# Performance work log

Measured on AMD Instinct MI355X. Metric: run time of the kernel, lower is better.

## Reference

```python
import jax, jax.numpy as jnp
import numpy as np

NHID = 512
T_K, T_Q, B = 256, 128, 8


def setup_inputs() -> dict:
    key = jax.random.key(0)
    k1, k2, k3, k4, k5 = jax.random.split(key, 5)
    query = jax.random.normal(k1, (T_Q, B, NHID), dtype=jnp.float32)
    c_key = jax.random.normal(k2, (T_K, B, NHID), dtype=jnp.float32)
    mask = jax.random.randint(k3, (T_K, B), 0, 2).astype(bool)
    # att_mlp params: Linear(2*nhid, nhid) -> Tanh -> Linear(nhid, 1)
    # stored as [in, out] so y = x @ W + b (torch Linear weight transposed)
    W1 = jax.random.normal(k4, (2 * NHID, NHID), dtype=jnp.float32) / np.sqrt(2 * NHID)
    b1 = jnp.zeros((NHID,), dtype=jnp.float32)
    W2 = jax.random.normal(k5, (NHID, 1), dtype=jnp.float32) / np.sqrt(NHID)
    b2 = jnp.zeros((1,), dtype=jnp.float32)
    return {"query": query, "c_key": c_key, "mask": mask,
            "W1": W1, "b1": b1, "W2": W2, "b2": b2}


def reference(query, c_key, mask, W1, b1, W2, b2):
    H = query.shape[-1]
    # cat([k_expand, q_expand], -1) @ W1 == k @ W1[:H] + q @ W1[H:]
    # (avoids materializing the [T_k, T_q, B, 2H] concat the torch code builds)
    k_proj = jnp.einsum('kbh,hd->kbd', c_key, W1[:H])   # [T_k, B, H]
    q_proj = jnp.einsum('qbh,hd->qbd', query, W1[H:])   # [T_q, B, H]
    h = jnp.tanh(k_proj[:, None, :, :] + q_proj[None, :, :, :] + b1)  # [T_k, T_q, B, H]
    att_score = jnp.einsum('kqbh,ho->kqb', h, W2) + b2[0]             # [T_k, T_q, B]
    att_score = jnp.where(mask[:, None, :], -jnp.inf, att_score)
    att_prob = jax.nn.softmax(att_score, axis=0)                      # softmax over keys
    # c_val defaults to c_key in the original forward
    ant_vec = jnp.einsum('kqb,kbh->qbh', att_prob, c_key)             # [T_q, B, H]
    return ant_vec, att_prob
```

## Files before the change

### kernel.cpp

```cpp
#include <hip/hip_runtime.h>
#include <math.h>

#define NHID 512
#define T_K  256
#define T_Q  128
#define BB   8

constexpr float C2L2E = 2.8853900817779268f;
constexpr float L2E   = 1.4426950408889634f;

__device__ __forceinline__ float fexp2(float x) { return __builtin_amdgcn_exp2f(x); }
__device__ __forceinline__ float frcp(float x)  { return __builtin_amdgcn_rcpf(x); }

typedef __attribute__((ext_vector_type(8))) short bf16x8;
typedef __attribute__((ext_vector_type(4))) float f32x4;
typedef __attribute__((ext_vector_type(2))) float f32x2;
typedef __attribute__((ext_vector_type(4))) float f32x4v;

__device__ __forceinline__ f32x2 fma2(f32x2 a, f32x2 b, f32x2 c) {
    return __builtin_elementwise_fma(a, b, c);
}

__device__ __forceinline__ unsigned short f2bf(float x) {
    unsigned u = __builtin_bit_cast(unsigned, x);
    unsigned r = (u + 0x7FFFu + ((u >> 16) & 1u)) >> 16;
    return (unsigned short)r;
}
__device__ __forceinline__ float bf2f(unsigned short h) {
    unsigned u = ((unsigned)h) << 16;
    return __builtin_bit_cast(float, u);
}
__device__ __forceinline__ unsigned packbf(float a, float b) {
    return (unsigned)f2bf(a) | ((unsigned)f2bf(b) << 16);
}
__device__ __forceinline__ float lo16(unsigned u) {
    return __builtin_bit_cast(float, u << 16);
}
__device__ __forceinline__ float hi16(unsigned u) {
    return __builtin_bit_cast(float, u & 0xFFFF0000u);
}

__global__ __launch_bounds__(256) void proj_kernel(
    const float* __restrict__ qry, const float* __restrict__ ckey,
    const float* __restrict__ W1, const float* __restrict__ b1,
    uint4* __restrict__ ekto, float* __restrict__ eq,
    unsigned int* __restrict__ ckp)
{
    const int row0 = blockIdx.x * 32;
    const int col0 = blockIdx.y * 64;
    const bool isK = row0 < 2048;
    const int bhalf = isK ? 0 : 512;

    __shared__ __align__(16) unsigned short As_h[32 * 64];
    __shared__ __align__(16) unsigned short As_l[32 * 64];
    __shared__ __align__(16) unsigned short Bs_h[64 * 64];
    __shared__ __align__(16) unsigned short Bs_l[64 * 64];

    const int t    = threadIdx.x;
    const int wave = t >> 6;
    const int lane = t & 63;
    const int wm = (wave & 1) * 16;
    const int wn = (wave >> 1) * 32;

    f32x4 acc[2] = {};

    const int srA = t >> 3;
    const int scA = (t & 7) * 8;
    const float* gA = (isK ? ckey + (size_t)(row0 + srA) * 512
                           : qry  + (size_t)(row0 - 2048 + srA) * 512) + scA;
    const int swA = ((scA >> 3) ^ (srA & 7)) * 8;
    const bool emit_ckp = isK && (col0 == 0);
    const int rowA = row0 + srA;
    unsigned int* ckp_dst = emit_ckp
        ? ckp + ((size_t)(rowA & 7) * 256 + (rowA >> 3)) * 256
        : nullptr;

    const int nB = t & 63;
    const int kgB = wave * 16;
    const float* gB = W1 + (size_t)(bhalf + kgB) * 512 + col0 + nB;
    const int caB = wave * 2;
    const int swB0 = nB * 64 + (((caB + 0) ^ (nB & 7)) * 8);
    const int swB1 = nB * 64 + (((caB + 1) ^ (nB & 7)) * 8);

    const int quad = lane >> 4, fr = lane & 15;

    float4 pa0 = *(const float4*)&gA[0];
    float4 pa1 = *(const float4*)&gA[4];
    float bv[16];
    #pragma unroll
    for (int kk = 0; kk < 16; ++kk)
        bv[kk] = gB[(size_t)kk * 512];

    for (int k0 = 0; k0 < 512; k0 += 64) {
        float fa[8];
        *(float4*)&fa[0] = pa0; *(float4*)&fa[4] = pa1;
        union { uint4 v; unsigned short s[8]; } hA, lA, bh0, bh1, bl0, bl1;
        #pragma unroll
        for (int e = 0; e < 8; ++e) {
            const unsigned short hb = f2bf(fa[e]);
            hA.s[e] = hb; lA.s[e] = f2bf(fa[e] - bf2f(hb));
        }
        #pragma unroll
        for (int e = 0; e < 8; ++e) {
            const unsigned short hb = f2bf(bv[e]);
            bh0.s[e] = hb; bl0.s[e] = f2bf(bv[e] - bf2f(hb));
        }
        #pragma unroll
        for (int e = 0; e < 8; ++e) {
            const unsigned short hb = f2bf(bv[8 + e]);
            bh1.s[e] = hb; bl1.s[e] = f2bf(bv[8 + e] - bf2f(hb));
        }
        if (emit_ckp)
            *(uint4*)&ckp_dst[(k0 + scA) >> 1] = hA.v;

        __syncthreads();
        *(uint4*)&As_h[srA * 64 + swA] = hA.v;
        *(uint4*)&As_l[srA * 64 + swA] = lA.v;
        *(uint4*)&Bs_h[swB0] = bh0.v;  *(uint4*)&Bs_h[swB1] = bh1.v;
        *(uint4*)&Bs_l[swB0] = bl0.v;  *(uint4*)&Bs_l[swB1] = bl1.v;
        __syncthreads();

        if (k0 + 64 < 512) {
            pa0 = *(const float4*)&gA[k0 + 64];
            pa1 = *(const float4*)&gA[k0 + 68];
            #pragma unroll
            for (int kk = 0; kk < 16; ++kk)
                bv[kk] = gB[(size_t)(k0 + 64 + kk) * 512];
        }

        #pragma unroll
        for (int ks = 0; ks < 2; ++ks) {
            const int cchunk = ks * 4 + quad;
            const int m = wm + fr;
            const bf16x8 afh = *(const bf16x8*)&As_h[m * 64 + ((cchunk ^ (m & 7)) * 8)];
            const bf16x8 afl = *(const bf16x8*)&As_l[m * 64 + ((cchunk ^ (m & 7)) * 8)];
            bf16x8 bfh[2], bfl[2];
            #pragma unroll
            for (int nt = 0; nt < 2; ++nt) {
                const int n = wn + nt * 16 + fr;
                bfh[nt] = *(const bf16x8*)&Bs_h[n * 64 + ((cchunk ^ (n & 7)) * 8)];
                bfl[nt] = *(const bf16x8*)&Bs_l[n * 64 + ((cchunk ^ (n & 7)) * 8)];
            }
            #pragma unroll
            for (int nt = 0; nt < 2; ++nt) {
                acc[nt] = __builtin_amdgcn_mfma_f32_16x16x32_bf16(afh, bfh[nt], acc[nt], 0, 0, 0);
                acc[nt] = __builtin_amdgcn_mfma_f32_16x16x32_bf16(afh, bfl[nt], acc[nt], 0, 0, 0);
                acc[nt] = __builtin_amdgcn_mfma_f32_16x16x32_bf16(afl, bfh[nt], acc[nt], 0, 0, 0);
            }
        }
    }

    #pragma unroll
    for (int nt = 0; nt < 2; ++nt) {
        const int colg = col0 + wn + nt * 16 + fr;
        const float b1v = b1[colg];
        #pragma unroll
        for (int i = 0; i < 4; ++i) {
            const int rowg = row0 + wm + quad * 4 + i;
            const float v = acc[nt][i];
            if (isK) {
                const float e = fexp2((v + b1v) * C2L2E);
                const float ep = __shfl_xor(e, 1, 64);
                unsigned pk = ((fr & 1) == 0) ? packbf(e, ep) : packbf(ep, e);
                unsigned pk2 = __shfl_xor(pk, 2, 64);
                if (fr & 2) { unsigned tmp = pk; pk = pk2; pk2 = tmp; }
                const unsigned px  = __shfl_xor(pk, 4, 64);
                const unsigned px2 = __shfl_xor(pk2, 4, 64);
                if ((fr & 7) == 0) {
                    const int kidx = rowg >> 3;
                    const int bb   = rowg & 7;
                    const int ho   = colg >> 3;
                    ekto[((size_t)bb * 64 + ho) * 256 + kidx] =
                        make_uint4(pk, pk2, px, px2);
                }
            } else {
                eq[(size_t)(rowg - 2048) * 512 + colg] = fexp2(v * C2L2E);
            }
        }
    }
}

__global__ __launch_bounds__(512, 4) void scoreav_kernel(
    const uint4* __restrict__ ekto, const float* __restrict__ eq,
    const float* __restrict__ W2, const float* __restrict__ b2,
    const int* __restrict__ mask, const unsigned int* __restrict__ ckp,
    float* __restrict__ prob_out, float* __restrict__ out_ant)
{
    const int t    = threadIdx.x;
    const int lane = t & 63;
    const int wave = __builtin_amdgcn_readfirstlane(t >> 6);
    const int hu   = __builtin_amdgcn_readfirstlane(t >> 8);
    const int kk   = t & 255;
    const int bid  = blockIdx.x;
    const int b    = bid & 7;
    const int q0   = (bid >> 3) * 2;

    __shared__ __align__(16) f32x2 eqp[512];
    __shared__ __align__(16) f32x2 rp2[512];
    __shared__ float ps[2][256];
    __shared__ __align__(8) f32x2 ps2[256];

    {
        const float* eqr0 = eq + ((size_t)q0 * 8 + b) * 512;
        const float* eqr1 = eq + ((size_t)(q0 + 1) * 8 + b) * 512;
        f32x2 ep; ep.x = eqr0[t]; ep.y = eqr1[t];
        eqp[t] = ep;
    }

    const float4 wA = *(const float4*)&W2[lane * 4];
    const float4 wB = *(const float4*)&W2[256 + lane * 4];
    float s2 = wA.x + wA.y + wA.z + wA.w + wB.x + wB.y + wB.z + wB.w;
    #pragma unroll
    for (int m = 32; m; m >>= 1) s2 += __shfl_xor(s2, m, 64);
    const float base = s2 + b2[0];
    __syncthreads();

    const uint4* __restrict__ ekb = ekto + (size_t)b * 64 * 256 + kk;
    const f32x2 one2 = {1.0f, 1.0f};
    f32x2 ra = {0.f, 0.f}, rb = {0.f, 0.f};

    uint4 LA0, LA1, LA2, LA3, LB0, LB1, LB2, LB3;

#define PREF(D, G) \
    D##0 = ekb[(size_t)(hu * 32 + (G) * 4 + 0) * 256]; \
    D##1 = ekb[(size_t)(hu * 32 + (G) * 4 + 1) * 256]; \
    D##2 = ekb[(size_t)(hu * 32 + (G) * 4 + 2) * 256]; \
    D##3 = ekb[(size_t)(hu * 32 + (G) * 4 + 3) * 256];

#define JBODY(U, G, J) { \
    const int hw = (hu * 32 + (G) * 4 + (J)) * 8; \
    const float ek0 = lo16(U.x), ek1 = hi16(U.x); \
    const float ek2 = lo16(U.y), ek3 = hi16(U.y); \
    const float ek4 = lo16(U.z), ek5 = hi16(U.z); \
    const float ek6 = lo16(U.w), ek7 = hi16(U.w); \
    const f32x4v E01 = *(const f32x4v*)&eqp[hw]; \
    const f32x4v E23 = *(const f32x4v*)&eqp[hw + 2]; \
    const f32x4v E45 = *(const f32x4v*)&eqp[hw + 4]; \
    const f32x4v E67 = *(const f32x4v*)&eqp[hw + 6]; \
    const float w0 = W2[hw + 0], w1 = W2[hw + 1]; \
    const float w2v = W2[hw + 2], w3 = W2[hw + 3]; \
    const float w4 = W2[hw + 4], w5 = W2[hw + 5]; \
    const float w6 = W2[hw + 6], w7 = W2[hw + 7]; \
    { \
        const f32x2 a0 = fma2((f32x2){ek0, ek0}, (f32x2){E01.x, E01.y}, one2); \
        const f32x2 a1 = fma2((f32x2){ek1, ek1}, (f32x2){E01.z, E01.w}, one2); \
        const f32x2 a2 = fma2((f32x2){ek2, ek2}, (f32x2){E23.x, E23.y}, one2); \
        const f32x2 a3 = fma2((f32x2){ek3, ek3}, (f32x2){E23.z, E23.w}, one2); \
        const f32x2 d01 = a0 * a1, d23 = a2 * a3; \
        const f32x2 n01 = fma2((f32x2){w0, w0}, a1, (f32x2){w1, w1} * a0); \
        const f32x2 n23 = fma2((f32x2){w2v, w2v}, a3, (f32x2){w3, w3} * a2); \
        const f32x2 N = fma2(n01, d23, n23 * d01); \
        const f32x2 D = d01 * d23; \
        const f32x2 R = {frcp(D.x), frcp(D.y)}; \
        ra = fma2(N, R, ra); \
    } \
    { \
        const f32x2 a0 = fma2((f32x2){ek4, ek4}, (f32x2){E45.x, E45.y}, one2); \
        const f32x2 a1 = fma2((f32x2){ek5, ek5}, (f32x2){E45.z, E45.w}, one2); \
        const f32x2 a2 = fma2((f32x2){ek6, ek6}, (f32x2){E67.x, E67.y}, one2); \
        const f32x2 a3 = fma2((f32x2){ek7, ek7}, (f32x2){E67.z, E67.w}, one2); \
        const f32x2 d01 = a0 * a1, d23 = a2 * a3; \
        const f32x2 n01 = fma2((f32x2){w4, w4}, a1, (f32x2){w5, w5} * a0); \
        const f32x2 n23 = fma2((f32x2){w6, w6}, a3, (f32x2){w7, w7} * a2); \
        const f32x2 N = fma2(n01, d23, n23 * d01); \
        const f32x2 D = d01 * d23; \
        const f32x2 R = {frcp(D.x), frcp(D.y)}; \
        rb = fma2(N, R, rb); \
    } \
}

#define GROUP(D, G) JBODY(D##0, G, 0) JBODY(D##1, G, 1) JBODY(D##2, G, 2) JBODY(D##3, G, 3)

    PREF(LA, 0)
    PREF(LB, 1) GROUP(LA, 0)
    PREF(LA, 2) GROUP(LB, 1)
    PREF(LB, 3) GROUP(LA, 2)
    PREF(LA, 4) GROUP(LB, 3)
    PREF(LB, 5) GROUP(LA, 4)
    PREF(LA, 6) GROUP(LB, 5)
    PREF(LB, 7) GROUP(LA, 6)
                GROUP(LB, 7)

#undef GROUP
#undef JBODY
#undef PREF

    rp2[t] = ra + rb;
    __syncthreads();

    if (t < 256) {
        const int msk = mask[t * 8 + b];
        const f32x2 rsum = rp2[t] + rp2[t + 256];
        float s0 = base - 2.0f * rsum.x;
        float s1 = base - 2.0f * rsum.y;
        if (msk) { s0 = -INFINITY; s1 = -INFINITY; }
        ps[0][t] = s0;
        ps[1][t] = s1;
    }
    __syncthreads();

    if (wave < 2) {
        float4 sv = *(const float4*)&ps[wave][lane * 4];
        float m = fmaxf(fmaxf(sv.x, sv.y), fmaxf(sv.z, sv.w));
        #pragma unroll
        for (int d = 32; d; d >>= 1) m = fmaxf(m, __shfl_xor(m, d, 64));
        float4 pv;
        pv.x = fexp2((sv.x - m) * L2E);
        pv.y = fexp2((sv.y - m) * L2E);
        pv.z = fexp2((sv.z - m) * L2E);
        pv.w = fexp2((sv.w - m) * L2E);
        float sum = pv.x + pv.y + pv.z + pv.w;
        #pragma unroll
        for (int d = 32; d; d >>= 1) sum += __shfl_xor(sum, d, 64);
        const float inv = frcp(sum);
        pv.x *= inv; pv.y *= inv; pv.z *= inv; pv.w *= inv;
        float* p2f = (float*)ps2;
        p2f[(lane * 4 + 0) * 2 + wave] = pv.x;
        p2f[(lane * 4 + 1) * 2 + wave] = pv.y;
        p2f[(lane * 4 + 2) * 2 + wave] = pv.z;
        p2f[(lane * 4 + 3) * 2 + wave] = pv.w;
        const int qb_idx = (q0 + wave) * 8 + b;
        const int kbase = lane * 4;
        prob_out[(size_t)(kbase + 0) * 1024 + qb_idx] = pv.x;
        prob_out[(size_t)(kbase + 1) * 1024 + qb_idx] = pv.y;
        prob_out[(size_t)(kbase + 2) * 1024 + qb_idx] = pv.z;
        prob_out[(size_t)(kbase + 3) * 1024 + qb_idx] = pv.w;
    }
    __syncthreads();

    {
        const int kq = lane >> 3;
        const int hq = lane & 7;
        const int pbase = wave * 32 + hq * 4;
        const unsigned int* __restrict__ ckb = ckp + (size_t)b * 256 * 256;
        f32x2 a0 = {}, a1 = {}, a2 = {}, a3 = {}, a4 = {}, a5 = {}, a6 = {}, a7 = {};
        #pragma unroll 8
        for (int ki = 0; ki < 32; ++ki) {
            const int k = ki * 8 + kq;
            const uint4 U = *(const uint4*)&ckb[(size_t)k * 256 + pbase];
            const float c0 = lo16(U.x), c1 = hi16(U.x);
            const float c2 = lo16(U.y), c3 = hi16(U.y);
            const float c4 = lo16(U.z), c5 = hi16(U.z);
            const float c6 = lo16(U.w), c7 = hi16(U.w);
            const f32x2 p = ps2[k];
            a0 = fma2(p, (f32x2){c0, c0}, a0);
            a1 = fma2(p, (f32x2){c1, c1}, a1);
            a2 = fma2(p, (f32x2){c2, c2}, a2);
            a3 = fma2(p, (f32x2){c3, c3}, a3);
            a4 = fma2(p, (f32x2){c4, c4}, a4);
            a5 = fma2(p, (f32x2){c5, c5}, a5);
            a6 = fma2(p, (f32x2){c6, c6}, a6);
            a7 = fma2(p, (f32x2){c7, c7}, a7);
        }
        #pragma unroll
        for (int d = 8; d <= 32; d <<= 1) {
            a0.x += __shfl_xor(a0.x, d, 64); a0.y += __shfl_xor(a0.y, d, 64);
            a1.x += __shfl_xor(a1.x, d, 64); a1.y += __shfl_xor(a1.y, d, 64);
            a2.x += __shfl_xor(a2.x, d, 64); a2.y += __shfl_xor(a2.y, d, 64);
            a3.x += __shfl_xor(a3.x, d, 64); a3.y += __shfl_xor(a3.y, d, 64);
            a4.x += __shfl_xor(a4.x, d, 64); a4.y += __shfl_xor(a4.y, d, 64);
            a5.x += __shfl_xor(a5.x, d, 64); a5.y += __shfl_xor(a5.y, d, 64);
            a6.x += __shfl_xor(a6.x, d, 64); a6.y += __shfl_xor(a6.y, d, 64);
            a7.x += __shfl_xor(a7.x, d, 64); a7.y += __shfl_xor(a7.y, d, 64);
        }
        if (lane < 8) {
            const int h0 = wave * 64 + hq * 8;
            float* o0 = &out_ant[((size_t)q0 * 8 + b) * 512 + h0];
            float* o1 = &out_ant[((size_t)(q0 + 1) * 8 + b) * 512 + h0];
            o0[0] = a0.x; o0[1] = a1.x; o0[2] = a2.x; o0[3] = a3.x;
            o0[4] = a4.x; o0[5] = a5.x; o0[6] = a6.x; o0[7] = a7.x;
            o1[0] = a0.y; o1[1] = a1.y; o1[2] = a2.y; o1[3] = a3.y;
            o1[4] = a4.y; o1[5] = a5.y; o1[6] = a6.y; o1[7] = a7.y;
        }
    }
}

extern "C" void kernel_launch(void* const* d_in, const int* in_sizes, int n_in,
                              void* d_out, int out_size, void* d_ws, size_t ws_size,
                              hipStream_t stream)
{
    const float* qry  = (const float*)d_in[0];
    const float* ckey = (const float*)d_in[1];
    const int*   mask = (const int*)d_in[2];
    const float* W1   = (const float*)d_in[3];
    const float* b1   = (const float*)d_in[4];
    const float* W2   = (const float*)d_in[5];
    const float* b2   = (const float*)d_in[6];

    float* out_ant  = (float*)d_out;
    float* out_prob = (float*)d_out + T_Q * BB * NHID;

    float* ws = (float*)d_ws;
    uint4* ws_ekto = (uint4*)ws;
    float* ws_eq  = ws + 524288;
    unsigned int* ws_ckp = (unsigned int*)(ws + 1048576);

    proj_kernel<<<dim3(96, 8), 256, 0, stream>>>(qry, ckey, W1, b1,
                                                 ws_ekto, ws_eq, ws_ckp);
    scoreav_kernel<<<dim3(512), 512, 0, stream>>>(ws_ekto, ws_eq, W2, b2, mask, ws_ckp,
                                                  out_prob, out_ant);
}
```

Baseline: 110.8 us.

## Pre-split operands to bf16 tiles and process four queries per score block

A new prep kernel converts the query, key and W1 inputs once into pre-swizzled bf16 hi/lo tiles. The projection GEMM then streams those tiles into double-buffered shared memory with a single barrier per step, instead of re-splitting the fp32 data in every block. The score/attention kernel now handles four queries per block instead of two, so each key-projection load and each c_key load serves twice as many queries. This halves the grid to 256 blocks and lowers the occupancy hint, and it adds a third kernel launch plus extra workspace traffic for the pre-split tiles.

```diff
diff --git a/kernel.cpp b/kernel.cpp
--- a/kernel.cpp
+++ b/kernel.cpp
@@ -40,106 +40,138 @@
     return __builtin_bit_cast(float, u & 0xFFFF0000u);
 }
 
-__global__ __launch_bounds__(256) void proj_kernel(
+__global__ __launch_bounds__(256) void prep_kernel(
     const float* __restrict__ qry, const float* __restrict__ ckey,
-    const float* __restrict__ W1, const float* __restrict__ b1,
-    uint4* __restrict__ ekto, float* __restrict__ eq,
+    const float* __restrict__ W1,
+    unsigned short* __restrict__ ash, unsigned short* __restrict__ asl,
+    unsigned short* __restrict__ w1h, unsigned short* __restrict__ w1l,
     unsigned int* __restrict__ ckp)
 {
-    const int row0 = blockIdx.x * 32;
-    const int col0 = blockIdx.y * 64;
+    const int t   = threadIdx.x;
+    const int bid = blockIdx.x;
+    if (bid < 96) {
+        const int rb = bid;
+        const int r  = t >> 3;
+        const int ca = t & 7;
+        const int row = rb * 32 + r;
+        const float* src = (row < 2048) ? (ckey + (size_t)row * 512)
+                                        : (qry + (size_t)(row - 2048) * 512);
+        const int swoff = r * 64 + ((ca ^ (r & 7)) * 8);
+        unsigned short* dh = ash + (size_t)rb * 8 * 2048;
+        unsigned short* dl = asl + (size_t)rb * 8 * 2048;
+        unsigned int* ckpd = (row < 2048)
+            ? ckp + ((size_t)(row & 7) * 256 + (row >> 3)) * 256
+            : nullptr;
+        #pragma unroll
+        for (int kc = 0; kc < 8; ++kc) {
+            const float4 f0 = *(const float4*)&src[kc * 64 + ca * 8];
+            const float4 f1 = *(const float4*)&src[kc * 64 + ca * 8 + 4];
+            float fa[8];
+            *(float4*)&fa[0] = f0; *(float4*)&fa[4] = f1;
+            union { uint4 v; unsigned short s[8]; } hv, lv;
+            #pragma unroll
+            for (int e = 0; e < 8; ++e) {
+                const unsigned short hb = f2bf(fa[e]);
+                hv.s[e] = hb; lv.s[e] = f2bf(fa[e] - bf2f(hb));
+            }
+            *(uint4*)&dh[kc * 2048 + swoff] = hv.v;
+            *(uint4*)&dl[kc * 2048 + swoff] = lv.v;
+            if (ckpd)
+                *(uint4*)&ckpd[kc * 32 + ca * 4] = hv.v;
+        }
+    } else {
+        const int tid = bid - 96;
+        const int h  = tid >> 6;
+        const int c0 = (tid >> 3) & 7;
+        const int kc = tid & 7;
+        const int n  = t & 63;
+        const int w  = t >> 6;
+        const float* gB = W1 + ((size_t)(h * 512 + kc * 64)) * 512 + c0 * 64 + n;
+        unsigned short* dh = w1h + (size_t)tid * 4096;
+        unsigned short* dl = w1l + (size_t)tid * 4096;
+        #pragma unroll
+        for (int g = 0; g < 2; ++g) {
+            const int cc = w * 2 + g;
+            float bv[8];
+            #pragma unroll
+            for (int e = 0; e < 8; ++e)
+                bv[e] = gB[(size_t)(cc * 8 + e) * 512];
+            union { uint4 v; unsigned short s[8]; } hv, lv;
+            #pragma unroll
+            for (int e = 0; e < 8; ++e) {
+                const unsigned short hb = f2bf(bv[e]);
+                hv.s[e] = hb; lv.s[e] = f2bf(bv[e] - bf2f(hb));
+            }
+            const int off = n * 64 + ((cc ^ (n & 7)) * 8);
+            *(uint4*)&dh[off] = hv.v;
+            *(uint4*)&dl[off] = lv.v;
+        }
+    }
+}
+
+__global__ __launch_bounds__(256) void proj_kernel(
+    const unsigned short* __restrict__ ash, const unsigned short* __restrict__ asl,
+    const unsigned short* __restrict__ w1h, const unsigned short* __restrict__ w1l,
+    const float* __restrict__ b1,
+    uint4* __restrict__ ekto, float* __restrict__ eq)
+{
+    const int bx = blockIdx.x, by = blockIdx.y;
+    const int row0 = bx * 32;
     const bool isK = row0 < 2048;
-    const int bhalf = isK ? 0 : 512;
-
-    __shared__ __align__(16) unsigned short As_h[32 * 64];
-    __shared__ __align__(16) unsigned short As_l[32 * 64];
-    __shared__ __align__(16) unsigned short Bs_h[64 * 64];
-    __shared__ __align__(16) unsigned short Bs_l[64 * 64];
+    const int h = isK ? 0 : 1;
+    const int col0 = by * 64;
+
+    __shared__ __align__(16) unsigned short As_h[2][2048];
+    __shared__ __align__(16) unsigned short As_l[2][2048];
+    __shared__ __align__(16) unsigned short Bs_h[2][4096];
+    __shared__ __align__(16) unsigned short Bs_l[2][4096];
 
     const int t    = threadIdx.x;
     const int wave = t >> 6;
     const int lane = t & 63;
     const int wm = (wave & 1) * 16;
     const int wn = (wave >> 1) * 32;
+    const int quad = lane >> 4, fr = lane & 15;
 
     f32x4 acc[2] = {};
 
-    const int srA = t >> 3;
-    const int scA = (t & 7) * 8;
-    const float* gA = (isK ? ckey + (size_t)(row0 + srA) * 512
-                           : qry  + (size_t)(row0 - 2048 + srA) * 512) + scA;
-    const int swA = ((scA >> 3) ^ (srA & 7)) * 8;
-    const bool emit_ckp = isK && (col0 == 0);
-    const int rowA = row0 + srA;
-    unsigned int* ckp_dst = emit_ckp
-        ? ckp + ((size_t)(rowA & 7) * 256 + (rowA >> 3)) * 256
-        : nullptr;
-
-    const int nB = t & 63;
-    const int kgB = wave * 16;
-    const float* gB = W1 + (size_t)(bhalf + kgB) * 512 + col0 + nB;
-    const int caB = wave * 2;
-    const int swB0 = nB * 64 + (((caB + 0) ^ (nB & 7)) * 8);
-    const int swB1 = nB * 64 + (((caB + 1) ^ (nB & 7)) * 8);
-
-    const int quad = lane >> 4, fr = lane & 15;
-
-    float4 pa0 = *(const float4*)&gA[0];
-    float4 pa1 = *(const float4*)&gA[4];
-    float bv[16];
-    #pragma unroll
-    for (int kk = 0; kk < 16; ++kk)
-        bv[kk] = gB[(size_t)kk * 512];
-
-    for (int k0 = 0; k0 < 512; k0 += 64) {
-        float fa[8];
-        *(float4*)&fa[0] = pa0; *(float4*)&fa[4] = pa1;
-        union { uint4 v; unsigned short s[8]; } hA, lA, bh0, bh1, bl0, bl1;
-        #pragma unroll
-        for (int e = 0; e < 8; ++e) {
-            const unsigned short hb = f2bf(fa[e]);
-            hA.s[e] = hb; lA.s[e] = f2bf(fa[e] - bf2f(hb));
-        }
-        #pragma unroll
-        for (int e = 0; e < 8; ++e) {
-            const unsigned short hb = f2bf(bv[e]);
-            bh0.s[e] = hb; bl0.s[e] = f2bf(bv[e] - bf2f(hb));
-        }
-        #pragma unroll
-        for (int e = 0; e < 8; ++e) {
-            const unsigned short hb = f2bf(bv[8 + e]);
-            bh1.s[e] = hb; bl1.s[e] = f2bf(bv[8 + e] - bf2f(hb));
-        }
-        if (emit_ckp)
-            *(uint4*)&ckp_dst[(k0 + scA) >> 1] = hA.v;
-
+    const uint4* ah = (const uint4*)ash + (size_t)bx * 8 * 256;
+    const uint4* al = (const uint4*)asl + (size_t)bx * 8 * 256;
+    const int tidB = (h * 8 + by) * 8;
+    const uint4* bh = (const uint4*)w1h + (size_t)tidB * 512;
+    const uint4* bl = (const uint4*)w1l + (size_t)tidB * 512;
+
+    uint4 rAh = ah[t], rAl = al[t];
+    uint4 rBh0 = bh[t], rBh1 = bh[256 + t];
+    uint4 rBl0 = bl[t], rBl1 = bl[256 + t];
+
+    for (int kc = 0; kc < 8; ++kc) {
+        const int cur = kc & 1;
+        *(uint4*)&As_h[cur][t * 8] = rAh;
+        *(uint4*)&As_l[cur][t * 8] = rAl;
+        *(uint4*)&Bs_h[cur][t * 8] = rBh0;
+        *(uint4*)&Bs_h[cur][2048 + t * 8] = rBh1;
+        *(uint4*)&Bs_l[cur][t * 8] = rBl0;
+        *(uint4*)&Bs_l[cur][2048 + t * 8] = rBl1;
         __syncthreads();
-        *(uint4*)&As_h[srA * 64 + swA] = hA.v;
-        *(uint4*)&As_l[srA * 64 + swA] = lA.v;
-        *(uint4*)&Bs_h[swB0] = bh0.v;  *(uint4*)&Bs_h[swB1] = bh1.v;
-        *(uint4*)&Bs_l[swB0] = bl0.v;  *(uint4*)&Bs_l[swB1] = bl1.v;
-        __syncthreads();
-
-        if (k0 + 64 < 512) {
-            pa0 = *(const float4*)&gA[k0 + 64];
-            pa1 = *(const float4*)&gA[k0 + 68];
-            #pragma unroll
-            for (int kk = 0; kk < 16; ++kk)
-                bv[kk] = gB[(size_t)(k0 + 64 + kk) * 512];
-        }
-
+        if (kc < 7) {
+            const int nx = kc + 1;
+            rAh = ah[nx * 256 + t];  rAl = al[nx * 256 + t];
+            rBh0 = bh[nx * 512 + t]; rBh1 = bh[nx * 512 + 256 + t];
+            rBl0 = bl[nx * 512 + t]; rBl1 = bl[nx * 512 + 256 + t];
+        }
         #pragma unroll
         for (int ks = 0; ks < 2; ++ks) {
             const int cchunk = ks * 4 + quad;
             const int m = wm + fr;
-            const bf16x8 afh = *(const bf16x8*)&As_h[m * 64 + ((cchunk ^ (m & 7)) * 8)];
-            const bf16x8 afl = *(const bf16x8*)&As_l[m * 64 + ((cchunk ^ (m & 7)) * 8)];
+            const bf16x8 afh = *(const bf16x8*)&As_h[cur][m * 64 + ((cchunk ^ (m & 7)) * 8)];
+            const bf16x8 afl = *(const bf16x8*)&As_l[cur][m * 64 + ((cchunk ^ (m & 7)) * 8)];
             bf16x8 bfh[2], bfl[2];
             #pragma unroll
             for (int nt = 0; nt < 2; ++nt) {
                 const int n = wn + nt * 16 + fr;
-                bfh[nt] = *(const bf16x8*)&Bs_h[n * 64 + ((cchunk ^ (n & 7)) * 8)];
-                bfl[nt] = *(const bf16x8*)&Bs_l[n * 64 + ((cchunk ^ (n & 7)) * 8)];
+                bfh[nt] = *(const bf16x8*)&Bs_h[cur][n * 64 + ((cchunk ^ (n & 7)) * 8)];
+                bfl[nt] = *(const bf16x8*)&Bs_l[cur][n * 64 + ((cchunk ^ (n & 7)) * 8)];
             }
             #pragma unroll
             for (int nt = 0; nt < 2; ++nt) {
@@ -180,7 +212,7 @@
     }
 }
 
-__global__ __launch_bounds__(512, 4) void scoreav_kernel(
+__global__ __launch_bounds__(512, 2) void scoreav_kernel(
     const uint4* __restrict__ ekto, const float* __restrict__ eq,
     const float* __restrict__ W2, const float* __restrict__ b2,
     const int* __restrict__ mask, const unsigned int* __restrict__ ckp,
@@ -193,18 +225,21 @@
     const int kk   = t & 255;
     const int bid  = blockIdx.x;
     const int b    = bid & 7;
-    const int q0   = (bid >> 3) * 2;
-
-    __shared__ __align__(16) f32x2 eqp[512];
-    __shared__ __align__(16) f32x2 rp2[512];
-    __shared__ float ps[2][256];
-    __shared__ __align__(8) f32x2 ps2[256];
+    const int q0   = (bid >> 3) * 4;
+
+    __shared__ __align__(16) f32x2 eqpA[512];
+    __shared__ __align__(16) f32x2 eqpB[512];
+    __shared__ __align__(16) f32x2 rpA[512];
+    __shared__ __align__(16) f32x2 rpB[512];
+    __shared__ float ps[4][256];
+    __shared__ __align__(8) f32x2 psA[256];
+    __shared__ __align__(8) f32x2 psB[256];
 
     {
-        const float* eqr0 = eq + ((size_t)q0 * 8 + b) * 512;
-        const float* eqr1 = eq + ((size_t)(q0 + 1) * 8 + b) * 512;
-        f32x2 ep; ep.x = eqr0[t]; ep.y = eqr1[t];
-        eqp[t] = ep;
+        const float* e0 = eq + ((size_t)q0 * 8 + b) * 512;
+        f32x2 va; va.x = e0[t];        va.y = e0[4096 + t];
+        f32x2 vb; vb.x = e0[8192 + t]; vb.y = e0[12288 + t];
+        eqpA[t] = va; eqpB[t] = vb;
     }
 
     const float4 wA = *(const float4*)&W2[lane * 4];
@@ -217,7 +252,8 @@
 
     const uint4* __restrict__ ekb = ekto + (size_t)b * 64 * 256 + kk;
     const f32x2 one2 = {1.0f, 1.0f};
-    f32x2 ra = {0.f, 0.f}, rb = {0.f, 0.f};
+    f32x2 raA = {0.f, 0.f}, rbA = {0.f, 0.f};
+    f32x2 raB = {0.f, 0.f}, rbB = {0.f, 0.f};
 
     uint4 LA0, LA1, LA2, LA3, LB0, LB1, LB2, LB3;
 
@@ -226,6 +262,20 @@
     D##1 = ekb[(size_t)(hu * 32 + (G) * 4 + 1) * 256]; \
     D##2 = ekb[(size_t)(hu * 32 + (G) * 4 + 2) * 256]; \
     D##3 = ekb[(size_t)(hu * 32 + (G) * 4 + 3) * 256];
+
+#define RAT(eka, ekb_, ekc, ekd, E01, E23, wx, wy, wz, ww, ACC) { \
+    const f32x2 a0 = fma2((f32x2){eka, eka}, (f32x2){E01.x, E01.y}, one2); \
+    const f32x2 a1 = fma2((f32x2){ekb_, ekb_}, (f32x2){E01.z, E01.w}, one2); \
+    const f32x2 a2 = fma2((f32x2){ekc, ekc}, (f32x2){E23.x, E23.y}, one2); \
+    const f32x2 a3 = fma2((f32x2){ekd, ekd}, (f32x2){E23.z, E23.w}, one2); \
+    const f32x2 d01 = a0 * a1, d23 = a2 * a3; \
+    const f32x2 n01 = fma2((f32x2){wx, wx}, a1, (f32x2){wy, wy} * a0); \
+    const f32x2 n23 = fma2((f32x2){wz, wz}, a3, (f32x2){ww, ww} * a2); \
+    const f32x2 N = fma2(n01, d23, n23 * d01); \
+    const f32x2 D = d01 * d23; \
+    const f32x2 R = {frcp(D.x), frcp(D.y)}; \
+    ACC = fma2(N, R, ACC); \
+}
 
 #define JBODY(U, G, J) { \
     const int hw = (hu * 32 + (G) * 4 + (J)) * 8; \
@@ -233,40 +283,22 @@
     const float ek2 = lo16(U.y), ek3 = hi16(U.y); \
     const float ek4 = lo16(U.z), ek5 = hi16(U.z); \
     const float ek6 = lo16(U.w), ek7 = hi16(U.w); \
-    const f32x4v E01 = *(const f32x4v*)&eqp[hw]; \
-    const f32x4v E23 = *(const f32x4v*)&eqp[hw + 2]; \
-    const f32x4v E45 = *(const f32x4v*)&eqp[hw + 4]; \
-    const f32x4v E67 = *(const f32x4v*)&eqp[hw + 6]; \
+    const f32x4v EA01 = *(const f32x4v*)&eqpA[hw]; \
+    const f32x4v EA23 = *(const f32x4v*)&eqpA[hw + 2]; \
+    const f32x4v EA45 = *(const f32x4v*)&eqpA[hw + 4]; \
+    const f32x4v EA67 = *(const f32x4v*)&eqpA[hw + 6]; \
+    const f32x4v EB01 = *(const f32x4v*)&eqpB[hw]; \
+    const f32x4v EB23 = *(const f32x4v*)&eqpB[hw + 2]; \
+    const f32x4v EB45 = *(const f32x4v*)&eqpB[hw + 4]; \
+    const f32x4v EB67 = *(const f32x4v*)&eqpB[hw + 6]; \
     const float w0 = W2[hw + 0], w1 = W2[hw + 1]; \
     const float w2v = W2[hw + 2], w3 = W2[hw + 3]; \
     const float w4 = W2[hw + 4], w5 = W2[hw + 5]; \
     const float w6 = W2[hw + 6], w7 = W2[hw + 7]; \
-    { \
-        const f32x2 a0 = fma2((f32x2){ek0, ek0}, (f32x2){E01.x, E01.y}, one2); \
-        const f32x2 a1 = fma2((f32x2){ek1, ek1}, (f32x2){E01.z, E01.w}, one2); \
-        const f32x2 a2 = fma2((f32x2){ek2, ek2}, (f32x2){E23.x, E23.y}, one2); \
-        const f32x2 a3 = fma2((f32x2){ek3, ek3}, (f32x2){E23.z, E23.w}, one2); \
-        const f32x2 d01 = a0 * a1, d23 = a2 * a3; \
-        const f32x2 n01 = fma2((f32x2){w0, w0}, a1, (f32x2){w1, w1} * a0); \
-        const f32x2 n23 = fma2((f32x2){w2v, w2v}, a3, (f32x2){w3, w3} * a2); \
-        const f32x2 N = fma2(n01, d23, n23 * d01); \
-        const f32x2 D = d01 * d23; \
-        const f32x2 R = {frcp(D.x), frcp(D.y)}; \
-        ra = fma2(N, R, ra); \
-    } \
-    { \
-        const f32x2 a0 = fma2((f32x2){ek4, ek4}, (f32x2){E45.x, E45.y}, one2); \
-        const f32x2 a1 = fma2((f32x2){ek5, ek5}, (f32x2){E45.z, E45.w}, one2); \
-        const f32x2 a2 = fma2((f32x2){ek6, ek6}, (f32x2){E67.x, E67.y}, one2); \
-        const f32x2 a3 = fma2((f32x2){ek7, ek7}, (f32x2){E67.z, E67.w}, one2); \
-        const f32x2 d01 = a0 * a1, d23 = a2 * a3; \
-        const f32x2 n01 = fma2((f32x2){w4, w4}, a1, (f32x2){w5, w5} * a0); \
-        const f32x2 n23 = fma2((f32x2){w6, w6}, a3, (f32x2){w7, w7} * a2); \
-        const f32x2 N = fma2(n01, d23, n23 * d01); \
-        const f32x2 D = d01 * d23; \
-        const f32x2 R = {frcp(D.x), frcp(D.y)}; \
-        rb = fma2(N, R, rb); \
-    } \
+    RAT(ek0, ek1, ek2, ek3, EA01, EA23, w0, w1, w2v, w3, raA) \
+    RAT(ek4, ek5, ek6, ek7, EA45, EA67, w4, w5, w6, w7, rbA) \
+    RAT(ek0, ek1, ek2, ek3, EB01, EB23, w0, w1, w2v, w3, raB) \
+    RAT(ek4, ek5, ek6, ek7, EB45, EB67, w4, w5, w6, w7, rbB) \
 }
 
 #define GROUP(D, G) JBODY(D##0, G, 0) JBODY(D##1, G, 1) JBODY(D##2, G, 2) JBODY(D##3, G, 3)
@@ -283,23 +315,27 @@
 
 #undef GROUP
 #undef JBODY
+#undef RAT
 #undef PREF
 
-    rp2[t] = ra + rb;
+    rpA[t] = raA + rbA;
+    rpB[t] = raB + rbB;
     __syncthreads();
 
     if (t < 256) {
         const int msk = mask[t * 8 + b];
-        const f32x2 rsum = rp2[t] + rp2[t + 256];
-        float s0 = base - 2.0f * rsum.x;
-        float s1 = base - 2.0f * rsum.y;
-        if (msk) { s0 = -INFINITY; s1 = -INFINITY; }
-        ps[0][t] = s0;
-        ps[1][t] = s1;
+        const f32x2 rsA = rpA[t] + rpA[t + 256];
+        const f32x2 rsB = rpB[t] + rpB[t + 256];
+        float s0 = base - 2.0f * rsA.x;
+        float s1 = base - 2.0f * rsA.y;
+        float s2_ = base - 2.0f * rsB.x;
+        float s3 = base - 2.0f * rsB.y;
+        if (msk) { s0 = -INFINITY; s1 = -INFINITY; s2_ = -INFINITY; s3 = -INFINITY; }
+        ps[0][t] = s0; ps[1][t] = s1; ps[2][t] = s2_; ps[3][t] = s3;
     }
     __syncthreads();
 
-    if (wave < 2) {
+    if (wave < 4) {
         float4 sv = *(const float4*)&ps[wave][lane * 4];
         float m = fmaxf(fmaxf(sv.x, sv.y), fmaxf(sv.z, sv.w));
         #pragma unroll
@@ -314,11 +350,12 @@
         for (int d = 32; d; d >>= 1) sum += __shfl_xor(sum, d, 64);
         const float inv = frcp(sum);
         pv.x *= inv; pv.y *= inv; pv.z *= inv; pv.w *= inv;
-        float* p2f = (float*)ps2;
-        p2f[(lane * 4 + 0) * 2 + wave] = pv.x;
-        p2f[(lane * 4 + 1) * 2 + wave] = pv.y;
-        p2f[(lane * 4 + 2) * 2 + wave] = pv.z;
-        p2f[(lane * 4 + 3) * 2 + wave] = pv.w;
+        float* pf = (wave < 2) ? (float*)psA : (float*)psB;
+        const int c = wave & 1;
+        pf[(lane * 4 + 0) * 2 + c] = pv.x;
+        pf[(lane * 4 + 1) * 2 + c] = pv.y;
+        pf[(lane * 4 + 2) * 2 + c] = pv.z;
+        pf[(lane * 4 + 3) * 2 + c] = pv.w;
         const int qb_idx = (q0 + wave) * 8 + b;
         const int kbase = lane * 4;
         prob_out[(size_t)(kbase + 0) * 1024 + qb_idx] = pv.x;
@@ -333,7 +370,8 @@
         const int hq = lane & 7;
         const int pbase = wave * 32 + hq * 4;
         const unsigned int* __restrict__ ckb = ckp + (size_t)b * 256 * 256;
-        f32x2 a0 = {}, a1 = {}, a2 = {}, a3 = {}, a4 = {}, a5 = {}, a6 = {}, a7 = {};
+        f32x2 aA0 = {}, aA1 = {}, aA2 = {}, aA3 = {}, aA4 = {}, aA5 = {}, aA6 = {}, aA7 = {};
+        f32x2 aB0 = {}, aB1 = {}, aB2 = {}, aB3 = {}, aB4 = {}, aB5 = {}, aB6 = {}, aB7 = {};
         #pragma unroll 8
         for (int ki = 0; ki < 32; ++ki) {
             const int k = ki * 8 + kq;
@@ -342,35 +380,38 @@
             const float c2 = lo16(U.y), c3 = hi16(U.y);
             const float c4 = lo16(U.z), c5 = hi16(U.z);
             const float c6 = lo16(U.w), c7 = hi16(U.w);
-            const f32x2 p = ps2[k];
-            a0 = fma2(p, (f32x2){c0, c0}, a0);
-            a1 = fma2(p, (f32x2){c1, c1}, a1);
-            a2 = fma2(p, (f32x2){c2, c2}, a2);
-            a3 = fma2(p, (f32x2){c3, c3}, a3);
-            a4 = fma2(p, (f32x2){c4, c4}, a4);
-            a5 = fma2(p, (f32x2){c5, c5}, a5);
-            a6 = fma2(p, (f32x2){c6, c6}, a6);
-            a7 = fma2(p, (f32x2){c7, c7}, a7);
-        }
+            const f32x2 pA = psA[k];
+            const f32x2 pB = psB[k];
+            aA0 = fma2(pA, (f32x2){c0, c0}, aA0); aB0 = fma2(pB, (f32x2){c0, c0}, aB0);
+            aA1 = fma2(pA, (f32x2){c1, c1}, aA1); aB1 = fma2(pB, (f32x2){c1, c1}, aB1);
+            aA2 = fma2(pA, (f32x2){c2, c2}, aA2); aB2 = fma2(pB, (f32x2){c2, c2}, aB2);
+            aA3 = fma2(pA, (f32x2){c3, c3}, aA3); aB3 = fma2(pB, (f32x2){c3, c3}, aB3);
+            aA4 = fma2(pA, (f32x2){c4, c4}, aA4); aB4 = fma2(pB, (f32x2){c4, c4}, aB4);
+            aA5 = fma2(pA, (f32x2){c5, c5}, aA5); aB5 = fma2(pB, (f32x2){c5, c5}, aB5);
+            aA6 = fma2(pA, (f32x2){c6, c6}, aA6); aB6 = fma2(pB, (f32x2){c6, c6}, aB6);
+            aA7 = fma2(pA, (f32x2){c7, c7}, aA7); aB7 = fma2(pB, (f32x2){c7, c7}, aB7);
+        }
+#define RED(v) { v.x += __shfl_xor(v.x, d, 64); v.y += __shfl_xor(v.y, d, 64); }
         #pragma unroll
         for (int d = 8; d <= 32; d <<= 1) {
-            a0.x += __shfl_xor(a0.x, d, 64); a0.y += __shfl_xor(a0.y, d, 64);
-            a1.x += __shfl_xor(a1.x, d, 64); a1.y += __shfl_xor(a1.y, d, 64);
-            a2.x += __shfl_xor(a2.x, d, 64); a2.y += __shfl_xor(a2.y, d, 64);
-            a3.x += __shfl_xor(a3.x, d, 64); a3.y += __shfl_xor(a3.y, d, 64);
-            a4.x += __shfl_xor(a4.x, d, 64); a4.y += __shfl_xor(a4.y, d, 64);
-            a5.x += __shfl_xor(a5.x, d, 64); a5.y += __shfl_xor(a5.y, d, 64);
-            a6.x += __shfl_xor(a6.x, d, 64); a6.y += __shfl_xor(a6.y, d, 64);
-            a7.x += __shfl_xor(a7.x, d, 64); a7.y += __shfl_xor(a7.y, d, 64);
-        }
+            RED(aA0) RED(aA1) RED(aA2) RED(aA3) RED(aA4) RED(aA5) RED(aA6) RED(aA7)
+            RED(aB0) RED(aB1) RED(aB2) RED(aB3) RED(aB4) RED(aB5) RED(aB6) RED(aB7)
+        }
+#undef RED
         if (lane < 8) {
             const int h0 = wave * 64 + hq * 8;
-            float* o0 = &out_ant[((size_t)q0 * 8 + b) * 512 + h0];
+            float* o0 = &out_ant[((size_t)(q0 + 0) * 8 + b) * 512 + h0];
             float* o1 = &out_ant[((size_t)(q0 + 1) * 8 + b) * 512 + h0];
-            o0[0] = a0.x; o0[1] = a1.x; o0[2] = a2.x; o0[3] = a3.x;
-            o0[4] = a4.x; o0[5] = a5.x; o0[6] = a6.x; o0[7] = a7.x;
-            o1[0] = a0.y; o1[1] = a1.y; o1[2] = a2.y; o1[3] = a3.y;
-            o1[4] = a4.y; o1[5] = a5.y; o1[6] = a6.y; o1[7] = a7.y;
+            float* o2 = &out_ant[((size_t)(q0 + 2) * 8 + b) * 512 + h0];
+            float* o3 = &out_ant[((size_t)(q0 + 3) * 8 + b) * 512 + h0];
+            o0[0] = aA0.x; o0[1] = aA1.x; o0[2] = aA2.x; o0[3] = aA3.x;
+            o0[4] = aA4.x; o0[5] = aA5.x; o0[6] = aA6.x; o0[7] = aA7.x;
+            o1[0] = aA0.y; o1[1] = aA1.y; o1[2] = aA2.y; o1[3] = aA3.y;
+            o1[4] = aA4.y; o1[5] = aA5.y; o1[6] = aA6.y; o1[7] = aA7.y;
+            o2[0] = aB0.x; o2[1] = aB1.x; o2[2] = aB2.x; o2[3] = aB3.x;
+            o2[4] = aB4.x; o2[5] = aB5.x; o2[6] = aB6.x; o2[7] = aB7.x;
+            o3[0] = aB0.y; o3[1] = aB1.y; o3[2] = aB2.y; o3[3] = aB3.y;
+            o3[4] = aB4.y; o3[5] = aB5.y; o3[6] = aB6.y; o3[7] = aB7.y;
         }
     }
 }
@@ -392,11 +433,17 @@
 
     float* ws = (float*)d_ws;
     uint4* ws_ekto = (uint4*)ws;
-    float* ws_eq  = ws + 524288;
+    float* ws_eq   = ws + 524288;
     unsigned int* ws_ckp = (unsigned int*)(ws + 1048576);
-
-    proj_kernel<<<dim3(96, 8), 256, 0, stream>>>(qry, ckey, W1, b1,
-                                                 ws_ekto, ws_eq, ws_ckp);
-    scoreav_kernel<<<dim3(512), 512, 0, stream>>>(ws_ekto, ws_eq, W2, b2, mask, ws_ckp,
+    unsigned short* ws_w1h = (unsigned short*)(ws + 1572864);
+    unsigned short* ws_w1l = (unsigned short*)(ws + 1835008);
+    unsigned short* ws_ash = (unsigned short*)(ws + 2097152);
+    unsigned short* ws_asl = (unsigned short*)(ws + 2883584);
+
+    prep_kernel<<<dim3(224), 256, 0, stream>>>(qry, ckey, W1,
+                                               ws_ash, ws_asl, ws_w1h, ws_w1l, ws_ckp);
+    proj_kernel<<<dim3(96, 8), 256, 0, stream>>>(ws_ash, ws_asl, ws_w1h, ws_w1l,
+                                                 b1, ws_ekto, ws_eq);
+    scoreav_kernel<<<dim3(256), 512, 0, stream>>>(ws_ekto, ws_eq, W2, b2, mask, ws_ckp,
                                                   out_prob, out_ant);
 }
```

Measured after the change: 114.8 us. 1.04x slower.
